# Kernel tuning notes

Measured on AMD Instinct MI355X. Metric: run time of the kernel, lower is better.

The kernel has to match this reference:

```python
import jax, jax.numpy as jnp
import numpy as np

B, S, D = 4, 2048, 1024  # batch, seq_len, model dim (= qk_dim = output_dim)


def setup_inputs() -> dict:
    key = jax.random.key(0)
    kq, kk, kv, kwq, kwk, kwv = jax.random.split(key, 6)
    q = jax.random.normal(kq, (B, S, D), dtype=jnp.float32)
    k = jax.random.normal(kk, (B, S, D), dtype=jnp.float32)
    v = jax.random.normal(kv, (B, S, D), dtype=jnp.float32)
    # causal mask, broadcast over batch
    mask = jnp.broadcast_to(jnp.tril(jnp.ones((S, S), dtype=bool)), (B, S, S))
    W_q = jax.random.uniform(kwq, (D, D), dtype=jnp.float32)
    W_k = jax.random.uniform(kwk, (D, D), dtype=jnp.float32)
    W_v = jax.random.uniform(kwv, (D, D), dtype=jnp.float32)
    return {"q": q, "k": k, "v": v, "mask": mask, "W_q": W_q, "W_k": W_k, "W_v": W_v}


def reference(q, k, v, mask, W_q, W_k, W_v):
    q1 = q @ W_q  # (B, S, D)
    k1 = k @ W_k  # (B, S, D)
    v1 = v @ W_v  # (B, S, D)
    qk = jnp.einsum('bij,bkj->bik', q1, k1)  # (B, S, S)
    qk = qk * jax.lax.rsqrt(float(k1.shape[-1]))
    neg_inf = jnp.finfo(jnp.float32).min
    qk = jnp.where(mask, qk, neg_inf)
    s = jax.nn.softmax(qk, axis=-1)
    return jnp.einsum('bij,bjk->bik', s, v1)
```

## Files before the change

### kernel.cpp

```cpp
#include <hip/hip_runtime.h>
#include <hip/hip_bf16.h>
#include <float.h>


typedef __attribute__((ext_vector_type(8))) short bf16x8;
typedef __attribute__((ext_vector_type(4))) float f32x4;

#define MFMA16 __builtin_amdgcn_mfma_f32_16x16x32_bf16

union U8 { bf16x8 v; unsigned w[4]; };

__device__ __forceinline__ ushort f2bf(float x) {
  union { float f; unsigned u; } v; v.f = x;
  unsigned r = v.u + 0x7fffu + ((v.u >> 16) & 1u);
  return (ushort)(r >> 16);
}
__device__ __forceinline__ float bf2f(ushort h) {
  union { unsigned u; float f; } v; v.u = ((unsigned)h) << 16;
  return v.f;
}
__device__ __forceinline__ void splitf(float x, ushort& hi, ushort& lo) {
  hi = f2bf(x);
  lo = f2bf(x - bf2f(hi));
}

__device__ __forceinline__ bf16x8 cvt8(const float* lp) {
  U8 H;
#pragma unroll
  for (int p = 0; p < 4; ++p) {
    const unsigned u0 = __float_as_uint(lp[2 * p]);
    const unsigned u1 = __float_as_uint(lp[2 * p + 1]);
    const unsigned r0 = (u0 + 0x7fffu + ((u0 >> 16) & 1u)) >> 16;
    const unsigned r1 = (u1 + 0x7fffu + ((u1 >> 16) & 1u)) & 0xffff0000u;
    H.w[p] = r0 | r1;
  }
  return H.v;
}

#define GLOAD16(gp, lp)                                                        \
  __builtin_amdgcn_global_load_lds(                                            \
      (const __attribute__((address_space(1))) void*)(gp),                     \
      (__attribute__((address_space(3))) void*)(lp), 16, 0, 0)

#define BARRIER() asm volatile("s_barrier" ::: "memory")
#define VMCNT8() asm volatile("s_waitcnt vmcnt(8)" ::: "memory")

__device__ __forceinline__ void stage_bf16_32(const ushort* g, int pitch,
                                              ushort* lds, int w, int lane) {
#pragma unroll
  for (int i = 0; i < 2; ++i) {
    const int c = w * 2 + i;
    const int row = c * 16 + (lane >> 2);
    const int kp = (lane & 3) * 8;
    GLOAD16(g + (size_t)row * pitch + kp, lds + c * 512);
  }
}
__device__ __forceinline__ void stage_bf16_64(const ushort* g, int pitch,
                                              ushort* lds, int w, int lane) {
#pragma unroll
  for (int i = 0; i < 4; ++i) {
    const int c = w * 4 + i;
    const int row = c * 8 + (lane >> 3);
    const int kp = (lane & 7) * 8;
    GLOAD16(g + (size_t)row * pitch + kp, lds + c * 512);
  }
}
__device__ __forceinline__ void stage_bf16_64x64(const ushort* g, int pitch,
                                                 ushort* lds, int w, int lane) {
#pragma unroll
  for (int i = 0; i < 2; ++i) {
    const int c = w * 2 + i;
    const int row = c * 8 + (lane >> 3);
    const int kp = (lane & 7) * 8;
    GLOAD16(g + (size_t)row * pitch + kp, lds + c * 512);
  }
}
__device__ __forceinline__ void stage_f32_32(const float* g, int pitch,
                                             float* lds, int w, int lane) {
#pragma unroll
  for (int i = 0; i < 4; ++i) {
    const int c = w * 4 + i;
    const int row = c * 8 + (lane >> 3);
    const int kp = (lane & 7) * 4;
    GLOAD16(g + (size_t)row * pitch + kp, lds + c * 256);
  }
}

__device__ __forceinline__ void stage_half8(const ushort* __restrict__ g,
                                            ushort* lds, int k0, int t) {
#pragma unroll
  for (int i = 0; i < 2; ++i) {
    const int c = t + i * 512;
    const int row = c >> 3;
    const int pcb = (c & 7) * 16;
    const int lcb = pcb ^ ((row & 7) << 4);
    GLOAD16(g + (size_t)row * 1024 + k0 + (lcb >> 1), lds + c * 8);
  }
}

__global__ __launch_bounds__(256) void wt_split(
    const float* __restrict__ q, const float* __restrict__ k,
    const float* __restrict__ W0, const float* __restrict__ W1,
    const float* __restrict__ W2, ushort* __restrict__ Th0,
    ushort* __restrict__ Tl0, ushort* __restrict__ Th1,
    ushort* __restrict__ Tl1, ushort* __restrict__ Th2,
    ushort* __restrict__ qh, ushort* __restrict__ ql,
    ushort* __restrict__ kh, ushort* __restrict__ kl) {
  __shared__ float t[32][33];
  const int f = blockIdx.x;
  if (f < 3072) {
    const int z = f >> 10, r10 = f & 1023;
    const int bx = r10 & 31, by = r10 >> 5;
    const float* W = z == 0 ? W0 : (z == 1 ? W1 : W2);
    ushort* Th = z == 0 ? Th0 : (z == 1 ? Th1 : Th2);
    ushort* Tl = z == 0 ? Tl0 : (z == 1 ? Tl1 : nullptr);
    const int r = threadIdx.x >> 3, c4 = (threadIdx.x & 7) * 4;
    const float4 x = *reinterpret_cast<const float4*>(
        &W[(size_t)(bx * 32 + r) * 1024 + by * 32 + c4]);
    t[r][c4] = x.x; t[r][c4 + 1] = x.y; t[r][c4 + 2] = x.z; t[r][c4 + 3] = x.w;
    __syncthreads();
    ushort h[4], l[4];
#pragma unroll
    for (int j = 0; j < 4; ++j) splitf(t[c4 + j][r], h[j], l[j]);
    const size_t o = (size_t)(by * 32 + r) * 1024 + bx * 32 + c4;
    *reinterpret_cast<ushort4*>(&Th[o]) = ushort4{h[0], h[1], h[2], h[3]};
    if (Tl)
      *reinterpret_cast<ushort4*>(&Tl[o]) = ushort4{l[0], l[1], l[2], l[3]};
  } else {
    const int fl = f - 3072;
    const float* X = (fl >> 11) ? k : q;
    ushort* H = (fl >> 11) ? kh : qh;
    ushort* L = (fl >> 11) ? kl : ql;
    const int n4 = 2097152;
    for (int i = (fl & 2047) * 256 + threadIdx.x; i < n4; i += 2048 * 256) {
      const float4 x = reinterpret_cast<const float4*>(X)[i];
      ushort h0, l0, h1, l1, h2, l2, h3, l3;
      splitf(x.x, h0, l0); splitf(x.y, h1, l1);
      splitf(x.z, h2, l2); splitf(x.w, h3, l3);
      reinterpret_cast<ushort4*>(H)[i] = ushort4{h0, h1, h2, h3};
      reinterpret_cast<ushort4*>(L)[i] = ushort4{l0, l1, l2, l3};
    }
  }
}

__global__ __launch_bounds__(512, 2) void proj_qk8(
    const ushort* __restrict__ Ah0, const ushort* __restrict__ Al0,
    const ushort* __restrict__ Ah1, const ushort* __restrict__ Al1,
    const ushort* __restrict__ Bh0, const ushort* __restrict__ Bl0,
    const ushort* __restrict__ Bh1, const ushort* __restrict__ Bl1,
    ushort* __restrict__ Oh0, ushort* __restrict__ Ol0,
    ushort* __restrict__ Oh1, ushort* __restrict__ Ol1) {
  __shared__ ushort As[2][16384];
  __shared__ ushort Bs[2][16384];
  const int bid = blockIdx.x;
  const int fid = (bid & 7) * 32 + (bid >> 3);
  const int z = fid >> 7, r = fid & 127;
  const int yt = r >> 2, xt = r & 3;
  const ushort* Ah = z ? Ah1 : Ah0;
  const ushort* Al = z ? Al1 : Al0;
  const ushort* Bh = z ? Bh1 : Bh0;
  const ushort* Bl = z ? Bl1 : Bl0;
  ushort* Oh = z ? Oh1 : Oh0;
  ushort* Ol = z ? Ol1 : Ol0;
  const size_t am0 = (size_t)yt * 256 * 1024;
  const size_t bn0 = (size_t)xt * 256 * 1024;
  const int t = threadIdx.x;
  const int lane = t & 63, w = t >> 6;
  const int wm = w >> 2, wn = w & 3;
  const int lr = lane & 15, kg = lane >> 4;
  f32x4 acc[8][4] = {};
  bf16x8 Ar[4][2], Br[4][2];

  auto stage_tile = [&](int kt) {
    if (kt >= 48) kt -= 48;
    const int seg = kt >> 4;
    const int k0 = (kt & 15) * 64;
    const int slot = kt & 1;
    const ushort* ga = (seg == 1) ? Al : Ah;
    const ushort* gb = (seg == 2) ? Bl : Bh;
#pragma unroll
    for (int h = 0; h < 2; ++h)
      stage_half8(ga + am0 + (size_t)(h * 128) * 1024, &As[slot][h * 8192], k0, t);
#pragma unroll
    for (int h = 0; h < 2; ++h)
      stage_half8(gb + bn0 + (size_t)(h * 128) * 1024, &Bs[slot][h * 8192], k0, t);
  };
  auto loadA = [&](int slot, int mq) {
#pragma unroll
    for (int m = 0; m < 4; ++m)
#pragma unroll
      for (int ks = 0; ks < 2; ++ks) {
        const int row = wm * 128 + (mq * 4 + m) * 16 + lr;
        const int cb = (ks * 64 + kg * 16) ^ ((row & 7) << 4);
        Ar[m][ks] =
            *reinterpret_cast<const bf16x8*>(&As[slot][row * 64 + (cb >> 1)]);
      }
  };
  auto loadB = [&](int slot, int nq) {
#pragma unroll
    for (int n = 0; n < 2; ++n)
#pragma unroll
      for (int ks = 0; ks < 2; ++ks) {
        const int col = wn * 64 + (nq * 2 + n) * 16 + lr;
        const int cb = (ks * 64 + kg * 16) ^ ((col & 7) << 4);
        Br[nq * 2 + n][ks] =
            *reinterpret_cast<const bf16x8*>(&Bs[slot][col * 64 + (cb >> 1)]);
      }
  };
  auto mfma_q = [&](int mq, int nq) {
    __builtin_amdgcn_s_setprio(1);
#pragma unroll
    for (int m = 0; m < 4; ++m)
#pragma unroll
      for (int n = 0; n < 2; ++n)
#pragma unroll
        for (int ks = 0; ks < 2; ++ks)
          acc[mq * 4 + m][nq * 2 + n] = MFMA16(
              Ar[m][ks], Br[nq * 2 + n][ks], acc[mq * 4 + m][nq * 2 + n], 0, 0, 0);
    __builtin_amdgcn_s_setprio(0);
  };

  stage_tile(0);
#pragma unroll 2
  for (int kt = 0; kt < 48; ++kt) {
    const int slot = kt & 1;
    stage_tile(kt + 1);
    VMCNT8();
    BARRIER();
    loadA(slot, 0); loadB(slot, 0);
    mfma_q(0, 0);
    loadB(slot, 1);
    mfma_q(0, 1);
    loadA(slot, 1);
    mfma_q(1, 0);
    mfma_q(1, 1);
    BARRIER();
  }

#pragma unroll
  for (int m = 0; m < 8; ++m)
#pragma unroll
    for (int n = 0; n < 4; ++n)
#pragma unroll
      for (int reg = 0; reg < 4; ++reg) {
        const int gm = yt * 256 + wm * 128 + m * 16 + kg * 4 + reg;
        const int gn = xt * 256 + wn * 64 + n * 16 + lr;
        ushort h, l;
        splitf(acc[m][n][reg], h, l);
        Oh[(size_t)gm * 1024 + gn] = h;
        Ol[(size_t)gm * 1024 + gn] = l;
      }
}

__global__ __launch_bounds__(256) void qk2(
    const ushort* __restrict__ q1h, const ushort* __restrict__ q1l,
    const ushort* __restrict__ k1h, const ushort* __restrict__ k1l,
    float* __restrict__ scoresA, float* __restrict__ scoresB) {
  __shared__ ushort Ahs[4096], Als[4096], Bhs[4096], Bls[4096];
  const int f = blockIdx.x;
  const int s = (f & 7) * 136 + (f >> 3);
  const int z = s / 544;
  const int rem = s % 544;
  const int b = rem / 136;
  int p = rem % 136, ti = 0, accp = 0;
  while (accp + ti + 1 <= p) { accp += ti + 1; ++ti; }
  const int tj = p - accp;
  const int tid = threadIdx.x, lane = tid & 63, w = tid >> 6;
  const int wr = w >> 1, wc = w & 1;
  const int lr = lane & 15, kg = lane >> 4;
  const int kh0 = z * 512;
  const ushort* qh = q1h + ((size_t)b * 2048 + ti * 128) * 1024 + kh0;
  const ushort* ql = q1l + ((size_t)b * 2048 + ti * 128) * 1024 + kh0;
  const ushort* kh = k1h + ((size_t)b * 2048 + tj * 128) * 1024 + kh0;
  const ushort* kl = k1l + ((size_t)b * 2048 + tj * 128) * 1024 + kh0;
  f32x4 acc[4][4] = {};

  for (int k0 = 0; k0 < 512; k0 += 32) {
    stage_bf16_32(qh + k0, 1024, Ahs, w, lane);
    stage_bf16_32(ql + k0, 1024, Als, w, lane);
    stage_bf16_32(kh + k0, 1024, Bhs, w, lane);
    stage_bf16_32(kl + k0, 1024, Bls, w, lane);
    __syncthreads();
    bf16x8 ah[4], al[4], bh[4], bl[4];
#pragma unroll
    for (int m = 0; m < 4; ++m) {
      ah[m] = *reinterpret_cast<bf16x8*>(&Ahs[(wr * 64 + m * 16 + lr) * 32 + kg * 8]);
      al[m] = *reinterpret_cast<bf16x8*>(&Als[(wr * 64 + m * 16 + lr) * 32 + kg * 8]);
    }
#pragma unroll
    for (int n = 0; n < 4; ++n) {
      bh[n] = *reinterpret_cast<bf16x8*>(&Bhs[(wc * 64 + n * 16 + lr) * 32 + kg * 8]);
      bl[n] = *reinterpret_cast<bf16x8*>(&Bls[(wc * 64 + n * 16 + lr) * 32 + kg * 8]);
    }
#pragma unroll
    for (int m = 0; m < 4; ++m)
#pragma unroll
      for (int n = 0; n < 4; ++n) {
        acc[m][n] = MFMA16(ah[m], bh[n], acc[m][n], 0, 0, 0);
        acc[m][n] = MFMA16(ah[m], bl[n], acc[m][n], 0, 0, 0);
        acc[m][n] = MFMA16(al[m], bh[n], acc[m][n], 0, 0, 0);
      }
    __syncthreads();
  }
  const float sc = 0.03125f;
  float* st = (z ? scoresB : scoresA) + ((size_t)b * 136 + p) * 16384;
#pragma unroll
  for (int m = 0; m < 4; ++m)
#pragma unroll
    for (int n = 0; n < 4; ++n)
#pragma unroll
      for (int reg = 0; reg < 4; ++reg) {
        const int il = wr * 64 + m * 16 + kg * 4 + reg;
        const int jl = wc * 64 + n * 16 + lr;
        st[il * 128 + jl] = acc[m][n][reg] * sc;
      }
}

__global__ __launch_bounds__(256) void sm_projv(
    float* __restrict__ scoresA, const float* __restrict__ scoresB,
    const ushort* __restrict__ Wvt, const float* __restrict__ V,
    ushort* __restrict__ v1t) {
  __shared__ __align__(16) char smem[24576];
  const int tid = threadIdx.x, lane = tid & 63, w = tid >> 6;
  const int fg = blockIdx.x;
  if (fg < 8192) {
    float* red = reinterpret_cast<float*>(smem);
    const int b = fg >> 11, r = fg & 2047;
    const int ti = r >> 7, rl = r & 127, ncol = (ti + 1) * 128;
    const int valid = r + 1;
    const size_t tbase = ((size_t)b * 136 + (ti * (ti + 1)) / 2) * 16384;
    float* srowA = scoresA + tbase;
    const float* srowB = scoresB + tbase;

    float vals[2][4];
    float mx = -FLT_MAX;
#pragma unroll
    for (int c = 0; c < 2; ++c) {
      const int j = tid * 4 + c * 1024;
      const size_t o = (size_t)(j >> 7) * 16384 + rl * 128 + (j & 127);
      const float4 a = *reinterpret_cast<const float4*>(srowA + o);
      const float4 bb = *reinterpret_cast<const float4*>(srowB + o);
      vals[c][0] = (j + 0 < valid) ? a.x + bb.x : -FLT_MAX;
      vals[c][1] = (j + 1 < valid) ? a.y + bb.y : -FLT_MAX;
      vals[c][2] = (j + 2 < valid) ? a.z + bb.z : -FLT_MAX;
      vals[c][3] = (j + 3 < valid) ? a.w + bb.w : -FLT_MAX;
      mx = fmaxf(mx, fmaxf(fmaxf(vals[c][0], vals[c][1]),
                           fmaxf(vals[c][2], vals[c][3])));
    }
#pragma unroll
    for (int o = 32; o; o >>= 1) mx = fmaxf(mx, __shfl_xor(mx, o));
    if (lane == 0) red[w] = mx;
    __syncthreads();
    mx = fmaxf(fmaxf(red[0], red[1]), fmaxf(red[2], red[3]));

    float ex[2][4];
    float sum = 0.f;
#pragma unroll
    for (int c = 0; c < 2; ++c)
#pragma unroll
      for (int e = 0; e < 4; ++e) {
        const int j = tid * 4 + c * 1024 + e;
        ex[c][e] = (j < valid) ? __expf(vals[c][e] - mx) : 0.f;
        sum += ex[c][e];
      }
#pragma unroll
    for (int o = 32; o; o >>= 1) sum += __shfl_xor(sum, o);
    if (lane == 0) red[4 + w] = sum;
    __syncthreads();
    sum = red[4] + red[5] + red[6] + red[7];
    const float inv = 1.f / sum;
#pragma unroll
    for (int c = 0; c < 2; ++c) {
      const int j = tid * 4 + c * 1024;
      if (j < ncol) {
        ushort* pt =
            reinterpret_cast<ushort*>(srowA + (size_t)(j >> 7) * 16384);
        ushort4 pw;
        pw.x = f2bf(ex[c][0] * inv); pw.y = f2bf(ex[c][1] * inv);
        pw.z = f2bf(ex[c][2] * inv); pw.w = f2bf(ex[c][3] * inv);
        *reinterpret_cast<ushort4*>(&pt[rl * 256 + (j & 127)]) = pw;
      }
    }
  } else {
    ushort* Ahs = reinterpret_cast<ushort*>(smem);
    float* Bs = reinterpret_cast<float*>(smem + 8192);
    const int f2 = fg - 8192;
    const int yb = (f2 >> 3) & 7;
    const int xb = (f2 & 7) + ((f2 >> 6) << 3);
    const int wr = w >> 1, wc = w & 1;
    const int lr = lane & 15, kg = lane >> 4;
    const int m0 = yb * 128;
    const int n0 = xb * 128;
    f32x4 acc[4][4] = {};

    for (int k0 = 0; k0 < 1024; k0 += 32) {
      stage_bf16_32(Wvt + (size_t)m0 * 1024 + k0, 1024, Ahs, w, lane);
      stage_f32_32(V + (size_t)n0 * 1024 + k0, 1024, Bs, w, lane);
      __syncthreads();
      bf16x8 ah[4], bh[4];
#pragma unroll
      for (int m = 0; m < 4; ++m)
        ah[m] = *reinterpret_cast<bf16x8*>(
            &Ahs[(wr * 64 + m * 16 + lr) * 32 + kg * 8]);
#pragma unroll
      for (int n = 0; n < 4; ++n)
        bh[n] = cvt8(&Bs[(wc * 64 + n * 16 + lr) * 32 + kg * 8]);
#pragma unroll
      for (int m = 0; m < 4; ++m)
#pragma unroll
        for (int n = 0; n < 4; ++n)
          acc[m][n] = MFMA16(ah[m], bh[n], acc[m][n], 0, 0, 0);
      __syncthreads();
    }
#pragma unroll
    for (int m = 0; m < 4; ++m)
#pragma unroll
      for (int n = 0; n < 4; ++n)
#pragma unroll
        for (int reg = 0; reg < 4; ++reg) {
          const int gm = m0 + wr * 64 + m * 16 + kg * 4 + reg;
          const int gn = n0 + wc * 64 + n * 16 + lr;
          const int b = gn >> 11, jj = gn & 2047;
          v1t[((size_t)b << 21) + (size_t)gm * 2048 + jj] = f2bf(acc[m][n][reg]);
        }
  }
}

__global__ __launch_bounds__(256) void pv2(const float* __restrict__ scores,
                                           const ushort* __restrict__ v1t,
                                           float* __restrict__ out) {
  __shared__ ushort Ps[128 * 64], Vs[64 * 64];
  const int fl = blockIdx.x;
  const int s = (fl & 7) * 128 + (fl >> 3);
  const int b = s >> 8, rem = s & 255;
  const int ti = 15 - (rem >> 4);
  const int n0 = (rem & 15) * 64;
  const int tid = threadIdx.x, lane = tid & 63, w = tid >> 6;
  const int wr = w >> 1, wc = w & 1;
  const int lr = lane & 15, kg = lane >> 4;
  const int tri_ti = (ti * (ti + 1)) / 2;
  const ushort* vbase = v1t + ((size_t)b << 21) + (size_t)n0 * 2048;
  const int kend = (ti + 1) * 128;
  f32x4 acc[4][2] = {};

  for (int k0 = 0; k0 < kend; k0 += 64) {
    const ushort* pt = reinterpret_cast<const ushort*>(
        scores + ((size_t)b * 136 + tri_ti + (k0 >> 7)) * 16384);
    stage_bf16_64(pt + (k0 & 64), 256, Ps, w, lane);
    stage_bf16_64x64(vbase + k0, 2048, Vs, w, lane);
    __syncthreads();
#pragma unroll
    for (int t2 = 0; t2 < 2; ++t2) {
      bf16x8 pa[4], vb[2];
#pragma unroll
      for (int m = 0; m < 4; ++m)
        pa[m] = *reinterpret_cast<bf16x8*>(
            &Ps[(wr * 64 + m * 16 + lr) * 64 + t2 * 32 + kg * 8]);
#pragma unroll
      for (int n = 0; n < 2; ++n)
        vb[n] = *reinterpret_cast<bf16x8*>(
            &Vs[(wc * 32 + n * 16 + lr) * 64 + t2 * 32 + kg * 8]);
#pragma unroll
      for (int m = 0; m < 4; ++m)
#pragma unroll
        for (int n = 0; n < 2; ++n)
          acc[m][n] = MFMA16(pa[m], vb[n], acc[m][n], 0, 0, 0);
    }
    __syncthreads();
  }
#pragma unroll
  for (int m = 0; m < 4; ++m)
#pragma unroll
    for (int n = 0; n < 2; ++n)
#pragma unroll
      for (int reg = 0; reg < 4; ++reg) {
        const int gm = ti * 128 + wr * 64 + m * 16 + kg * 4 + reg;
        const int gn = n0 + wc * 32 + n * 16 + lr;
        out[((size_t)b * 2048 + gm) * 1024 + gn] = acc[m][n][reg];
      }
}

extern "C" void kernel_launch(void* const* d_in, const int* in_sizes, int n_in,
                              void* d_out, int out_size, void* d_ws,
                              size_t ws_size, hipStream_t stream) {
  const float* q = (const float*)d_in[0];
  const float* k = (const float*)d_in[1];
  const float* v = (const float*)d_in[2];
  const float* Wq = (const float*)d_in[4];
  const float* Wk = (const float*)d_in[5];
  const float* Wv = (const float*)d_in[6];
  float* out = (float*)d_out;

  char* ws = (char*)d_ws;
  const size_t SCORES_T = 35651584;
  float* scoresA = (float*)ws;
  float* scoresB = (float*)(ws + SCORES_T);
  ushort* qsh = (ushort*)ws;
  ushort* qsl = qsh + 8388608;
  ushort* ksh = qsh + 2 * 8388608;
  ushort* ksl = qsh + 3 * 8388608;
  ushort* q1hi = (ushort*)(ws + 2 * SCORES_T);
  ushort* q1lo = q1hi + 8388608;
  ushort* k1hi = q1hi + 2 * 8388608;
  ushort* k1lo = q1hi + 3 * 8388608;
  ushort* v1t = (ushort*)(ws + 2 * SCORES_T);
  ushort* Wqth = (ushort*)(ws + 2 * SCORES_T + 67108864);
  ushort* Wqtl = Wqth + 1048576;
  ushort* Wkth = Wqth + 2097152;
  ushort* Wktl = Wqth + 3145728;
  ushort* Wvt  = Wqth + 4194304;
  const size_t need = 2 * SCORES_T + 67108864 + 10485760;
  if (ws_size < need) return;

  dim3 blk(256);
  wt_split<<<dim3(7168), blk, 0, stream>>>(q, k, Wq, Wk, Wv, Wqth, Wqtl, Wkth,
                                           Wktl, Wvt, qsh, qsl, ksh, ksl);
  proj_qk8<<<dim3(256), dim3(512), 0, stream>>>(qsh, qsl, ksh, ksl, Wqth,
                                                Wqtl, Wkth, Wktl, q1hi, q1lo,
                                                k1hi, k1lo);
  qk2<<<dim3(1088), blk, 0, stream>>>(q1hi, q1lo, k1hi, k1lo, scoresA,
                                      scoresB);
  sm_projv<<<dim3(8704), blk, 0, stream>>>(scoresA, scoresB, Wvt, v, v1t);
  pv2<<<dim3(1024), blk, 0, stream>>>(scoresA, v1t, out);
}
```

Baseline: 308.7 us.

## Interleave per-quarter global-to-LDS staging with MFMA phases in split GEMM

Splits tile staging into four quarter-groups (two B halves, two A halves) and issues them one at a time between MFMA phases, with a deeper prefetch of six groups ahead. Extra barriers let each LDS slot region be overwritten only after its consumers have loaded their fragments, and the wait count drops to vmcnt(4). The aim is to spread memory traffic across the compute loop instead of bursting it at the top of each iteration. In exchange it adds many more s_barrier calls per iteration, which may stall waves.

```diff
diff --git a/kernel.cpp b/kernel.cpp
--- a/kernel.cpp
+++ b/kernel.cpp
@@ -43,7 +43,7 @@
       (__attribute__((address_space(3))) void*)(lp), 16, 0, 0)
 
 #define BARRIER() asm volatile("s_barrier" ::: "memory")
-#define VMCNT8() asm volatile("s_waitcnt vmcnt(8)" ::: "memory")
+#define VMCNT4() asm volatile("s_waitcnt vmcnt(4)" ::: "memory")
 
 __device__ __forceinline__ void stage_bf16_32(const ushort* g, int pitch,
                                               ushort* lds, int w, int lane) {
@@ -171,19 +171,20 @@
   f32x4 acc[8][4] = {};
   bf16x8 Ar[4][2], Br[4][2];
 
-  auto stage_tile = [&](int kt) {
-    if (kt >= 48) kt -= 48;
+  auto stageG = [&](int G) {
+    if (G >= 192) G -= 192;
+    const int kt = G >> 2, h = G & 3;
     const int seg = kt >> 4;
     const int k0 = (kt & 15) * 64;
     const int slot = kt & 1;
-    const ushort* ga = (seg == 1) ? Al : Ah;
-    const ushort* gb = (seg == 2) ? Bl : Bh;
-#pragma unroll
-    for (int h = 0; h < 2; ++h)
-      stage_half8(ga + am0 + (size_t)(h * 128) * 1024, &As[slot][h * 8192], k0, t);
-#pragma unroll
-    for (int h = 0; h < 2; ++h)
+    if (h < 2) {
+      const ushort* gb = (seg == 2) ? Bl : Bh;
       stage_half8(gb + bn0 + (size_t)(h * 128) * 1024, &Bs[slot][h * 8192], k0, t);
+    } else {
+      const int ah = h - 2;
+      const ushort* ga = (seg == 1) ? Al : Ah;
+      stage_half8(ga + am0 + (size_t)(ah * 128) * 1024, &As[slot][ah * 8192], k0, t);
+    }
   };
   auto loadA = [&](int slot, int mq) {
 #pragma unroll
@@ -220,19 +221,31 @@
     __builtin_amdgcn_s_setprio(0);
   };
 
-  stage_tile(0);
+#pragma unroll
+  for (int G = 0; G < 6; ++G) stageG(G);
+
 #pragma unroll 2
   for (int kt = 0; kt < 48; ++kt) {
     const int slot = kt & 1;
-    stage_tile(kt + 1);
-    VMCNT8();
+    const int P = 4 * kt;
+    stageG(P + 6);
+    VMCNT4();
     BARRIER();
     loadA(slot, 0); loadB(slot, 0);
     mfma_q(0, 0);
+    BARRIER();
     loadB(slot, 1);
+    stageG(P + 7);
+    BARRIER();
     mfma_q(0, 1);
+    BARRIER();
     loadA(slot, 1);
+    stageG(P + 8);
+    BARRIER();
     mfma_q(1, 0);
+    BARRIER();
+    stageG(P + 9);
+    BARRIER();
     mfma_q(1, 1);
     BARRIER();
   }
```

New measurement: 312.8 us. About the same (+1.3%).

## Share a pipelined 128x128 split-bf16 GEMM core between projection and QK kernels

Applied to the files above, without the earlier changes.

Adds a templated gemm128 routine with double-buffered global-to-LDS staging, XOR-swizzled LDS layout and the three split-precision products (hi*hi, hi*lo, lo*hi) run as sequential K segments. The QK projection moves from 256x256 tiles with 512 threads to 128x128 tiles with 256 threads over 1024 blocks, which raises block count for better CU fill but lowers per-block operand reuse. The QK score kernel drops its single-buffered, synchronised k-loop with four separate LDS arrays and uses the same pipelined core, aiming to overlap loads with MFMA and cut bank conflicts.

```diff
diff --git a/kernel.cpp b/kernel.cpp
--- a/kernel.cpp
+++ b/kernel.cpp
@@ -44,6 +44,7 @@
 
 #define BARRIER() asm volatile("s_barrier" ::: "memory")
 #define VMCNT8() asm volatile("s_waitcnt vmcnt(8)" ::: "memory")
+#define VMCNT0() asm volatile("s_waitcnt vmcnt(0)" ::: "memory")
 
 __device__ __forceinline__ void stage_bf16_32(const ushort* g, int pitch,
                                               ushort* lds, int w, int lane) {
@@ -86,15 +87,76 @@
   }
 }
 
-__device__ __forceinline__ void stage_half8(const ushort* __restrict__ g,
-                                            ushort* lds, int k0, int t) {
-#pragma unroll
-  for (int i = 0; i < 2; ++i) {
-    const int c = t + i * 512;
-    const int row = c >> 3;
-    const int pcb = (c & 7) * 16;
-    const int lcb = pcb ^ ((row & 7) << 4);
-    GLOAD16(g + (size_t)row * 1024 + k0 + (lcb >> 1), lds + c * 8);
+template <int NT, int TPS>
+__device__ __forceinline__ void gemm128(
+    const ushort* __restrict__ Ah, const ushort* __restrict__ Al,
+    const ushort* __restrict__ Bh, const ushort* __restrict__ Bl,
+    ushort (*As)[8192], ushort (*Bs)[8192], f32x4 (&acc)[4][4], int t) {
+  const int lane = t & 63, w = t >> 6;
+  const int wm = w >> 1, wn = w & 1;
+  const int lr = lane & 15, kg = lane >> 4;
+
+  auto stage_tile = [&](int kt) {
+    const int seg = kt / TPS;
+    const int k0 = (kt % TPS) * 64;
+    const int slot = kt & 1;
+    const ushort* ga = (seg == 1) ? Al : Ah;
+    const ushort* gb = (seg == 2) ? Bl : Bh;
+#pragma unroll
+    for (int i = 0; i < 4; ++i) {
+      const int c = t + i * 256;
+      const int row = c >> 3;
+      const int lcb = ((c & 7) * 16) ^ ((row & 7) << 4);
+      GLOAD16(ga + (size_t)row * 1024 + k0 + (lcb >> 1), As[slot] + c * 8);
+    }
+#pragma unroll
+    for (int i = 0; i < 4; ++i) {
+      const int c = t + i * 256;
+      const int row = c >> 3;
+      const int lcb = ((c & 7) * 16) ^ ((row & 7) << 4);
+      GLOAD16(gb + (size_t)row * 1024 + k0 + (lcb >> 1), Bs[slot] + c * 8);
+    }
+  };
+
+  stage_tile(0);
+  for (int kt = 0; kt < NT; ++kt) {
+    const int slot = kt & 1;
+    if (kt + 1 < NT) {
+      stage_tile(kt + 1);
+      VMCNT8();
+    } else {
+      VMCNT0();
+    }
+    BARRIER();
+    bf16x8 Ar[4][2], Br[4][2];
+#pragma unroll
+    for (int m = 0; m < 4; ++m)
+#pragma unroll
+      for (int ks = 0; ks < 2; ++ks) {
+        const int row = wm * 64 + m * 16 + lr;
+        const int cb = (ks * 64 + kg * 16) ^ ((row & 7) << 4);
+        Ar[m][ks] =
+            *reinterpret_cast<const bf16x8*>(&As[slot][row * 64 + (cb >> 1)]);
+      }
+#pragma unroll
+    for (int n = 0; n < 4; ++n)
+#pragma unroll
+      for (int ks = 0; ks < 2; ++ks) {
+        const int col = wn * 64 + n * 16 + lr;
+        const int cb = (ks * 64 + kg * 16) ^ ((col & 7) << 4);
+        Br[n][ks] =
+            *reinterpret_cast<const bf16x8*>(&Bs[slot][col * 64 + (cb >> 1)]);
+      }
+    __builtin_amdgcn_s_setprio(1);
+#pragma unroll
+    for (int m = 0; m < 4; ++m)
+#pragma unroll
+      for (int n = 0; n < 4; ++n)
+#pragma unroll
+        for (int ks = 0; ks < 2; ++ks)
+          acc[m][n] = MFMA16(Ar[m][ks], Br[n][ks], acc[m][n], 0, 0, 0);
+    __builtin_amdgcn_s_setprio(0);
+    BARRIER();
   }
 }
 
@@ -143,108 +205,40 @@
   }
 }
 
-__global__ __launch_bounds__(512, 2) void proj_qk8(
-    const ushort* __restrict__ Ah0, const ushort* __restrict__ Al0,
-    const ushort* __restrict__ Ah1, const ushort* __restrict__ Al1,
-    const ushort* __restrict__ Bh0, const ushort* __restrict__ Bl0,
-    const ushort* __restrict__ Bh1, const ushort* __restrict__ Bl1,
-    ushort* __restrict__ Oh0, ushort* __restrict__ Ol0,
-    ushort* __restrict__ Oh1, ushort* __restrict__ Ol1) {
-  __shared__ ushort As[2][16384];
-  __shared__ ushort Bs[2][16384];
+__global__ __launch_bounds__(256) void proj_qk12(
+    const ushort* __restrict__ qsh, const ushort* __restrict__ qsl,
+    const ushort* __restrict__ ksh, const ushort* __restrict__ ksl,
+    const ushort* __restrict__ Wqth, const ushort* __restrict__ Wqtl,
+    const ushort* __restrict__ Wkth, const ushort* __restrict__ Wktl,
+    ushort* __restrict__ q1hi, ushort* __restrict__ q1lo,
+    ushort* __restrict__ k1hi, ushort* __restrict__ k1lo) {
+  __shared__ ushort As[2][8192], Bs[2][8192];
   const int bid = blockIdx.x;
-  const int fid = (bid & 7) * 32 + (bid >> 3);
-  const int z = fid >> 7, r = fid & 127;
-  const int yt = r >> 2, xt = r & 3;
-  const ushort* Ah = z ? Ah1 : Ah0;
-  const ushort* Al = z ? Al1 : Al0;
-  const ushort* Bh = z ? Bh1 : Bh0;
-  const ushort* Bl = z ? Bl1 : Bl0;
-  ushort* Oh = z ? Oh1 : Oh0;
-  ushort* Ol = z ? Ol1 : Ol0;
-  const size_t am0 = (size_t)yt * 256 * 1024;
-  const size_t bn0 = (size_t)xt * 256 * 1024;
+  const int fid = (bid & 7) * 128 + (bid >> 3);
+  const int z = fid >> 9;
+  const int r = fid & 511;
+  const int yt = r >> 3, xt = r & 7;
+  const ushort* Ah = (z ? ksh : qsh) + (size_t)yt * 128 * 1024;
+  const ushort* Al = (z ? ksl : qsl) + (size_t)yt * 128 * 1024;
+  const ushort* Bh = (z ? Wkth : Wqth) + (size_t)xt * 128 * 1024;
+  const ushort* Bl = (z ? Wktl : Wqtl) + (size_t)xt * 128 * 1024;
+  ushort* Oh = z ? k1hi : q1hi;
+  ushort* Ol = z ? k1lo : q1lo;
   const int t = threadIdx.x;
+  f32x4 acc[4][4] = {};
+  gemm128<48, 16>(Ah, Al, Bh, Bl, As, Bs, acc, t);
+
   const int lane = t & 63, w = t >> 6;
-  const int wm = w >> 2, wn = w & 3;
+  const int wm = w >> 1, wn = w & 1;
   const int lr = lane & 15, kg = lane >> 4;
-  f32x4 acc[8][4] = {};
-  bf16x8 Ar[4][2], Br[4][2];
-
-  auto stage_tile = [&](int kt) {
-    if (kt >= 48) kt -= 48;
-    const int seg = kt >> 4;
-    const int k0 = (kt & 15) * 64;
-    const int slot = kt & 1;
-    const ushort* ga = (seg == 1) ? Al : Ah;
-    const ushort* gb = (seg == 2) ? Bl : Bh;
-#pragma unroll
-    for (int h = 0; h < 2; ++h)
-      stage_half8(ga + am0 + (size_t)(h * 128) * 1024, &As[slot][h * 8192], k0, t);
-#pragma unroll
-    for (int h = 0; h < 2; ++h)
-      stage_half8(gb + bn0 + (size_t)(h * 128) * 1024, &Bs[slot][h * 8192], k0, t);
-  };
-  auto loadA = [&](int slot, int mq) {
-#pragma unroll
-    for (int m = 0; m < 4; ++m)
-#pragma unroll
-      for (int ks = 0; ks < 2; ++ks) {
-        const int row = wm * 128 + (mq * 4 + m) * 16 + lr;
-        const int cb = (ks * 64 + kg * 16) ^ ((row & 7) << 4);
-        Ar[m][ks] =
-            *reinterpret_cast<const bf16x8*>(&As[slot][row * 64 + (cb >> 1)]);
-      }
-  };
-  auto loadB = [&](int slot, int nq) {
-#pragma unroll
-    for (int n = 0; n < 2; ++n)
-#pragma unroll
-      for (int ks = 0; ks < 2; ++ks) {
-        const int col = wn * 64 + (nq * 2 + n) * 16 + lr;
-        const int cb = (ks * 64 + kg * 16) ^ ((col & 7) << 4);
-        Br[nq * 2 + n][ks] =
-            *reinterpret_cast<const bf16x8*>(&Bs[slot][col * 64 + (cb >> 1)]);
-      }
-  };
-  auto mfma_q = [&](int mq, int nq) {
-    __builtin_amdgcn_s_setprio(1);
-#pragma unroll
-    for (int m = 0; m < 4; ++m)
-#pragma unroll
-      for (int n = 0; n < 2; ++n)
-#pragma unroll
-        for (int ks = 0; ks < 2; ++ks)
-          acc[mq * 4 + m][nq * 2 + n] = MFMA16(
-              Ar[m][ks], Br[nq * 2 + n][ks], acc[mq * 4 + m][nq * 2 + n], 0, 0, 0);
-    __builtin_amdgcn_s_setprio(0);
-  };
-
-  stage_tile(0);
-#pragma unroll 2
-  for (int kt = 0; kt < 48; ++kt) {
-    const int slot = kt & 1;
-    stage_tile(kt + 1);
-    VMCNT8();
-    BARRIER();
-    loadA(slot, 0); loadB(slot, 0);
-    mfma_q(0, 0);
-    loadB(slot, 1);
-    mfma_q(0, 1);
-    loadA(slot, 1);
-    mfma_q(1, 0);
-    mfma_q(1, 1);
-    BARRIER();
-  }
-
-#pragma unroll
-  for (int m = 0; m < 8; ++m)
+#pragma unroll
+  for (int m = 0; m < 4; ++m)
 #pragma unroll
     for (int n = 0; n < 4; ++n)
 #pragma unroll
       for (int reg = 0; reg < 4; ++reg) {
-        const int gm = yt * 256 + wm * 128 + m * 16 + kg * 4 + reg;
-        const int gn = xt * 256 + wn * 64 + n * 16 + lr;
+        const int gm = yt * 128 + wm * 64 + m * 16 + kg * 4 + reg;
+        const int gn = xt * 128 + wn * 64 + n * 16 + lr;
         ushort h, l;
         splitf(acc[m][n][reg], h, l);
         Oh[(size_t)gm * 1024 + gn] = h;
@@ -252,11 +246,11 @@
       }
 }
 
-__global__ __launch_bounds__(256) void qk2(
+__global__ __launch_bounds__(256) void qk12(
     const ushort* __restrict__ q1h, const ushort* __restrict__ q1l,
     const ushort* __restrict__ k1h, const ushort* __restrict__ k1l,
     float* __restrict__ scoresA, float* __restrict__ scoresB) {
-  __shared__ ushort Ahs[4096], Als[4096], Bhs[4096], Bls[4096];
+  __shared__ ushort As[2][8192], Bs[2][8192];
   const int f = blockIdx.x;
   const int s = (f & 7) * 136 + (f >> 3);
   const int z = s / 544;
@@ -265,43 +259,18 @@
   int p = rem % 136, ti = 0, accp = 0;
   while (accp + ti + 1 <= p) { accp += ti + 1; ++ti; }
   const int tj = p - accp;
-  const int tid = threadIdx.x, lane = tid & 63, w = tid >> 6;
-  const int wr = w >> 1, wc = w & 1;
-  const int lr = lane & 15, kg = lane >> 4;
   const int kh0 = z * 512;
   const ushort* qh = q1h + ((size_t)b * 2048 + ti * 128) * 1024 + kh0;
   const ushort* ql = q1l + ((size_t)b * 2048 + ti * 128) * 1024 + kh0;
   const ushort* kh = k1h + ((size_t)b * 2048 + tj * 128) * 1024 + kh0;
   const ushort* kl = k1l + ((size_t)b * 2048 + tj * 128) * 1024 + kh0;
+  const int t = threadIdx.x;
   f32x4 acc[4][4] = {};
-
-  for (int k0 = 0; k0 < 512; k0 += 32) {
-    stage_bf16_32(qh + k0, 1024, Ahs, w, lane);
-    stage_bf16_32(ql + k0, 1024, Als, w, lane);
-    stage_bf16_32(kh + k0, 1024, Bhs, w, lane);
-    stage_bf16_32(kl + k0, 1024, Bls, w, lane);
-    __syncthreads();
-    bf16x8 ah[4], al[4], bh[4], bl[4];
-#pragma unroll
-    for (int m = 0; m < 4; ++m) {
-      ah[m] = *reinterpret_cast<bf16x8*>(&Ahs[(wr * 64 + m * 16 + lr) * 32 + kg * 8]);
-      al[m] = *reinterpret_cast<bf16x8*>(&Als[(wr * 64 + m * 16 + lr) * 32 + kg * 8]);
-    }
-#pragma unroll
-    for (int n = 0; n < 4; ++n) {
-      bh[n] = *reinterpret_cast<bf16x8*>(&Bhs[(wc * 64 + n * 16 + lr) * 32 + kg * 8]);
-      bl[n] = *reinterpret_cast<bf16x8*>(&Bls[(wc * 64 + n * 16 + lr) * 32 + kg * 8]);
-    }
-#pragma unroll
-    for (int m = 0; m < 4; ++m)
-#pragma unroll
-      for (int n = 0; n < 4; ++n) {
-        acc[m][n] = MFMA16(ah[m], bh[n], acc[m][n], 0, 0, 0);
-        acc[m][n] = MFMA16(ah[m], bl[n], acc[m][n], 0, 0, 0);
-        acc[m][n] = MFMA16(al[m], bh[n], acc[m][n], 0, 0, 0);
-      }
-    __syncthreads();
-  }
+  gemm128<24, 8>(qh, ql, kh, kl, As, Bs, acc, t);
+
+  const int lane = t & 63, w = t >> 6;
+  const int wm = w >> 1, wn = w & 1;
+  const int lr = lane & 15, kg = lane >> 4;
   const float sc = 0.03125f;
   float* st = (z ? scoresB : scoresA) + ((size_t)b * 136 + p) * 16384;
 #pragma unroll
@@ -310,8 +279,8 @@
     for (int n = 0; n < 4; ++n)
 #pragma unroll
       for (int reg = 0; reg < 4; ++reg) {
-        const int il = wr * 64 + m * 16 + kg * 4 + reg;
-        const int jl = wc * 64 + n * 16 + lr;
+        const int il = wm * 64 + m * 16 + kg * 4 + reg;
+        const int jl = wn * 64 + n * 16 + lr;
         st[il * 128 + jl] = acc[m][n][reg] * sc;
       }
 }
@@ -515,11 +484,11 @@
   dim3 blk(256);
   wt_split<<<dim3(7168), blk, 0, stream>>>(q, k, Wq, Wk, Wv, Wqth, Wqtl, Wkth,
                                            Wktl, Wvt, qsh, qsl, ksh, ksl);
-  proj_qk8<<<dim3(256), dim3(512), 0, stream>>>(qsh, qsl, ksh, ksl, Wqth,
-                                                Wqtl, Wkth, Wktl, q1hi, q1lo,
-                                                k1hi, k1lo);
-  qk2<<<dim3(1088), blk, 0, stream>>>(q1hi, q1lo, k1hi, k1lo, scoresA,
-                                      scoresB);
+  proj_qk12<<<dim3(1024), blk, 0, stream>>>(qsh, qsl, ksh, ksl, Wqth, Wqtl,
+                                            Wkth, Wktl, q1hi, q1lo, k1hi,
+                                            k1lo);
+  qk12<<<dim3(1088), blk, 0, stream>>>(q1hi, q1lo, k1hi, k1lo, scoresA,
+                                       scoresB);
   sm_projv<<<dim3(8704), blk, 0, stream>>>(scoresA, scoresB, Wvt, v, v1t);
   pv2<<<dim3(1024), blk, 0, stream>>>(scoresA, v1t, out);
 }
```

Measured after the change: 342.3 us. 10.9% more time.
